# Kernel tuning notes

Hardware: AMD Instinct MI355X
Metric: run time of the kernel (lower is better)

Reference implementation:

```python
import jax, jax.numpy as jnp
import numpy as np

N, K, D, H, FF = 1024, 16, 512, 8, 2048
MUL_A, ES = 64, 64
E = N * K
HD = D // H          # vector channels per head
MH = MUL_A // H      # alpha channels per head
EPS = 1e-6


def smooth_lrelu(x, a=0.2):
    # SmoothLeakyReLU: (1+a)/2*x + (1-a)/2*x*(2*sigmoid(x)-1)
    return 0.5 * (1 + a) * x + 0.5 * (1 - a) * x * jnp.tanh(0.5 * x)


def vn_ln(x, g, b):
    # Vector-Neuron LayerNorm: LN over channel norms, rescale vectors.  x: [N, C, 3]
    n = jnp.sqrt(jnp.sum(x * x, axis=-1) + EPS)                  # [N, C]
    mu = n.mean(-1, keepdims=True)
    var = n.var(-1, keepdims=True)
    ln = (n - mu) / jnp.sqrt(var + EPS) * g + b
    return x / n[..., None] * ln[..., None]


def setup_inputs() -> dict:
    keys = iter(jax.random.split(jax.random.key(0), 40))
    def nrm(shape, scale=1.0):
        return jax.random.normal(next(keys), shape, jnp.float32) * scale
    d = {}
    d['tgt'] = nrm((N, 3 * D))
    d['memory'] = nrm((N, K, 3 * D))
    d['edge_sh'] = nrm((E, 4))
    d['edge_scalars'] = jax.random.uniform(next(keys), (E, ES), jnp.float32)
    sD = D ** -0.5
    d['W_src'] = nrm((D, D), sD)
    d['W_dst'] = nrm((D, D), sD)
    d['fc_w1'] = nrm((ES, 32), ES ** -0.5); d['fc_b1'] = jnp.zeros((32,), jnp.float32)
    d['fc_w2'] = nrm((32, 32), 32 ** -0.5); d['fc_b2'] = jnp.zeros((32,), jnp.float32)
    d['fc_w3'] = nrm((32, 3 * D), 32 ** -0.5); d['fc_b3'] = jnp.zeros((3 * D,), jnp.float32)
    d['W_alpha'] = nrm((D, MUL_A), sD)
    d['ln_a_g'] = jnp.ones((MUL_A,), jnp.float32)
    d['ln_a_b'] = jnp.zeros((MUL_A,), jnp.float32)
    d['alpha_dot'] = nrm((H, MH), MH ** -0.5)
    d['W_value'] = nrm((D, D), sD)
    d['W_proj'] = nrm((D, D), sD)
    d['n1_g'] = jnp.ones((D,), jnp.float32); d['n1_b'] = jnp.zeros((D,), jnp.float32)
    d['n2_g'] = jnp.ones((D,), jnp.float32); d['n2_b'] = jnp.zeros((D,), jnp.float32)
    d['W_ff1'] = nrm((FF, D), sD)
    d['W_ffd'] = nrm((FF, FF), FF ** -0.5)
    d['W_ff2'] = nrm((D, FF), FF ** -0.5)
    return d


def reference(tgt, memory, edge_sh, edge_scalars, W_src, W_dst,
              fc_w1, fc_b1, fc_w2, fc_b2, fc_w3, fc_b3,
              W_alpha, ln_a_g, ln_a_b, alpha_dot, W_value, W_proj,
              n1_g, n1_b, n2_g, n2_b, W_ff1, W_ffd, W_ff2):
    n, d3 = tgt.shape
    k = memory.shape[1]
    tv = jnp.einsum('oc,ncx->nox', W_dst, tgt.reshape(n, D, 3))          # linear_dst
    mv = jnp.einsum('oc,nkcx->nkox', W_src, memory.reshape(n, k, D, 3))  # linear_src
    msg = (tv[:, None] + mv).reshape(n * k, D, 3)                         # [E, D, 3]
    # radial MLP -> depthwise tensor-product weights
    h = jax.nn.silu(edge_scalars @ fc_w1 + fc_b1)
    h = jax.nn.silu(h @ fc_w2 + fc_b2)
    w = h @ fc_w3 + fc_b3                                                 # [E, 3D]
    w0, w1, w2 = jnp.split(w, 3, axis=-1)
    s = edge_sh[:, 0]
    v = edge_sh[:, 1:4]
    # depthwise TP with edge attr (1x0e+1x1e): 1e x 1e -> 0e, 1e x 0e -> 1e, 1e x 1e -> 1e
    p_sc = w0 * jnp.einsum('ecx,ex->ec', msg, v) / jnp.sqrt(3.0)          # [E, D]
    p_v1 = w1[:, :, None] * msg * s[:, None, None]                        # [E, D, 3]
    p_v2 = w2[:, :, None] * jnp.cross(msg, v[:, None, :]) / jnp.sqrt(2.0)
    # MLP attention on the invariant channel
    a = p_sc @ W_alpha                                                    # [E, MUL_A]
    a = (a - a.mean(-1, keepdims=True)) / jnp.sqrt(a.var(-1, keepdims=True) + EPS) * ln_a_g + ln_a_b
    a = smooth_lrelu(a).reshape(-1, H, MH)
    a = jnp.einsum('ehm,hm->eh', a, alpha_dot).reshape(n, k, H)
    a = jax.nn.softmax(a, axis=1)                                          # softmax over neighbors
    val = jnp.einsum('oc,ecx->eox', W_value, p_v1 + p_v2).reshape(n, k, H, HD, 3)
    out = jnp.einsum('nkh,nkhdx->nhdx', a, val).reshape(n, D, 3)
    out = jnp.einsum('oc,ncx->nox', W_proj, out)
    x = vn_ln(tv + out, n1_g, n1_b)
    # VN feed-forward: VNLinear -> VNLeakyReLU -> VNLinear
    y = jnp.einsum('oc,ncx->nox', W_ff1, x)                                # [N, FF, 3]
    dvec = jnp.einsum('oc,ncx->nox', W_ffd, y)
    dot = jnp.sum(y * dvec, -1)
    dnn = jnp.sum(dvec * dvec, -1) + EPS
    yproj = y - (dot / dnn)[..., None] * dvec
    y = jnp.where((dot >= 0)[..., None], y, 0.2 * y + 0.8 * yproj)
    y = jnp.einsum('oc,ncx->nox', W_ff2, y)
    x = vn_ln(x + y, n2_g, n2_b)
    return x.reshape(n, -1)
```

## Files before the change

### kernel.cpp

```cpp
#include <hip/hip_runtime.h>
#include <hip/hip_bf16.h>
#include <math.h>

#define EPS 1e-6f
#define RS3 0.57735026918962576f
#define RS2 0.70710678118654752f

typedef __attribute__((ext_vector_type(8))) short bf16x8;
typedef __attribute__((ext_vector_type(4))) float f32x4;

__device__ __forceinline__ ushort f2bf(float f) {
  unsigned u = __float_as_uint(f);
  u += 0x7fffu + ((u >> 16) & 1u);
  return (ushort)(u >> 16);
}
__device__ __forceinline__ float bf2f(ushort u) {
  return __uint_as_float(((unsigned)u) << 16);
}
__device__ __forceinline__ void split_hl(float v, ushort& h, ushort& l) {
  h = f2bf(v);
  l = f2bf(v - bf2f(h));
}
__device__ __forceinline__ float wave_sum64(float v) {
#pragma unroll
  for (int m = 32; m > 0; m >>= 1) v += __shfl_xor(v, m, 64);
  return v;
}

__global__ __launch_bounds__(256) void cvt_weights_hl(
    const float* __restrict__ w_src, const float* __restrict__ w_dst,
    const float* __restrict__ w_ff1, const float* __restrict__ w_ffd,
    const float* __restrict__ w_ff2, ushort* __restrict__ oh, ushort* __restrict__ ol)
{
  long i = ((long)blockIdx.x * 256 + threadIdx.x) * 8;
  const float* s; long l;
  if      (i < 262144)  { s = w_src; l = i; }
  else if (i < 524288)  { s = w_dst; l = i - 262144; }
  else if (i < 1572864) { s = w_ff1; l = i - 524288; }
  else if (i < 5767168) { s = w_ffd; l = i - 1572864; }
  else                  { s = w_ff2; l = i - 5767168; }
  ushort h[8], lo[8];
#pragma unroll
  for (int j = 0; j < 8; ++j) split_hl(s[l + j], h[j], lo[j]);
  ushort4 h0 = {h[0], h[1], h[2], h[3]}, h1 = {h[4], h[5], h[6], h[7]};
  ushort4 l0 = {lo[0], lo[1], lo[2], lo[3]}, l1 = {lo[4], lo[5], lo[6], lo[7]};
  *(ushort4*)(oh + i) = h0; *(ushort4*)(oh + i + 4) = h1;
  *(ushort4*)(ol + i) = l0; *(ushort4*)(ol + i + 4) = l1;
}

__global__ __launch_bounds__(256) void cvt_in_hl(
    const float* __restrict__ in, ushort* __restrict__ oh, ushort* __restrict__ ol)
{
  __shared__ float lds[6144];
  const int t = threadIdx.x;
  const long b0 = (long)blockIdx.x * 4;
  const float* ib = in + b0 * 1536;
#pragma unroll
  for (int r = 0; r < 6; ++r)
    *(float4*)(lds + r * 1024 + t * 4) = *(const float4*)(ib + r * 1024 + t * 4);
  __syncthreads();
#pragma unroll
  for (int r = 0; r < 24; ++r) {
    int l = t + 256 * r;
    int b = l >> 11, rem = l & 2047;
    b = l / 1536; rem = l - b * 1536;
    int x = rem >> 9, c = rem & 511;
    float v = lds[b * 1536 + c * 3 + x];
    ushort h, lo; split_hl(v, h, lo);
    oh[(b0 + b) * 1536 + rem] = h;
    ol[(b0 + b) * 1536 + rem] = lo;
  }
}

__global__ __launch_bounds__(256) void wcomb_kernel(
    const float* __restrict__ Wp, const float* __restrict__ Wv,
    ushort* __restrict__ oh, ushort* __restrict__ ol)
{
  __shared__ float wp[64 * 65];
  __shared__ float wv[64 * 65];
  const int h = blockIdx.x >> 3, ct = blockIdx.x & 7, pt = blockIdx.y;
  const int t = threadIdx.x;
#pragma unroll
  for (int r = 0; r < 16; ++r) {
    int f = r * 256 + t;
    int p = f >> 6, o = f & 63;
    wp[p * 65 + o] = Wp[(long)(pt * 64 + p) * 512 + h * 64 + o];
  }
#pragma unroll
  for (int r = 0; r < 16; ++r) {
    int f = r * 256 + t;
    int o = f >> 6, c = f & 63;
    wv[o * 65 + c] = Wv[(long)(h * 64 + o) * 512 + ct * 64 + c];
  }
  __syncthreads();
  const int tp = t >> 4, tc = t & 15;
  float acc[4][4] = {};
  for (int o = 0; o < 64; ++o) {
    float av[4], bv[4];
#pragma unroll
    for (int i = 0; i < 4; ++i) av[i] = wp[(tp * 4 + i) * 65 + o];
#pragma unroll
    for (int j = 0; j < 4; ++j) bv[j] = wv[o * 65 + tc * 4 + j];
#pragma unroll
    for (int i = 0; i < 4; ++i)
#pragma unroll
      for (int j = 0; j < 4; ++j) acc[i][j] += av[i] * bv[j];
  }
#pragma unroll
  for (int i = 0; i < 4; ++i) {
    int p = pt * 64 + tp * 4 + i;
    ushort h4[4], l4[4];
#pragma unroll
    for (int j = 0; j < 4; ++j) split_hl(acc[i][j], h4[j], l4[j]);
    ushort4 hv = {h4[0], h4[1], h4[2], h4[3]}, lv = {l4[0], l4[1], l4[2], l4[3]};
    long o = (long)p * 4096 + h * 512 + ct * 64 + tc * 4;
    *(ushort4*)(oh + o) = hv;
    *(ushort4*)(ol + o) = lv;
  }
}

template<int MT>
__global__ __launch_bounds__(256) void gemm_hl(
    const ushort* __restrict__ AH, const ushort* __restrict__ AL,
    const ushort* __restrict__ BH, const ushort* __restrict__ BL,
    float* __restrict__ Cf, ushort* __restrict__ CH, ushort* __restrict__ CL,
    const float* __restrict__ ADD, int M, int K, long bnp, int outmode)
{
  __shared__ __align__(16) ushort AsH[32 * MT * 72];
  __shared__ __align__(16) ushort AsL[32 * MT * 72];
  __shared__ __align__(16) ushort BsH[96 * 72];
  __shared__ __align__(16) ushort BsL[96 * 72];
  const int t = threadIdx.x;
  const int m0 = blockIdx.x * (32 * MT);
  const int j0 = blockIdx.y * 96;
  const int wid = t >> 6, lane = t & 63;
  const int wm = (wid >> 1) * (16 * MT), wn = (wid & 1) * 48;
  const int r16 = lane & 15, quad = lane >> 4;

  f32x4 acc[MT][3];
#pragma unroll
  for (int i = 0; i < MT; ++i)
#pragma unroll
    for (int j = 0; j < 3; ++j) acc[i][j] = (f32x4){0.f, 0.f, 0.f, 0.f};

  for (int k0 = 0; k0 < K; k0 += 64) {
#pragma unroll
    for (int r = 0; r < MT; ++r) {
      int f = r * 256 + t;
      int m = f >> 3, kc = f & 7;
      long off = (long)(m0 + m) * K + k0 + kc * 8;
      *(uint4*)(AsH + m * 72 + kc * 8) = *(const uint4*)(AH + off);
      *(uint4*)(AsL + m * 72 + kc * 8) = *(const uint4*)(AL + off);
    }
#pragma unroll
    for (int r = 0; r < 3; ++r) {
      int f = r * 256 + t;
      int n = f >> 3, kc = f & 7;
      int jj = j0 + n;
      int bq = jj / 3, xr = jj - bq * 3;
      long off = (long)bq * bnp + (long)xr * K + k0 + kc * 8;
      *(uint4*)(BsH + n * 72 + kc * 8) = *(const uint4*)(BH + off);
      *(uint4*)(BsL + n * 72 + kc * 8) = *(const uint4*)(BL + off);
    }
    __syncthreads();
#pragma unroll
    for (int kh = 0; kh < 2; ++kh) {
      bf16x8 ah[MT], al[MT], bh[3], bl[3];
#pragma unroll
      for (int i = 0; i < MT; ++i) {
        int ro = (wm + i * 16 + r16) * 72 + kh * 32 + quad * 8;
        ah[i] = *(const bf16x8*)(AsH + ro);
        al[i] = *(const bf16x8*)(AsL + ro);
      }
#pragma unroll
      for (int j = 0; j < 3; ++j) {
        int ro = (wn + j * 16 + r16) * 72 + kh * 32 + quad * 8;
        bh[j] = *(const bf16x8*)(BsH + ro);
        bl[j] = *(const bf16x8*)(BsL + ro);
      }
#pragma unroll
      for (int i = 0; i < MT; ++i)
#pragma unroll
        for (int j = 0; j < 3; ++j) {
          acc[i][j] = __builtin_amdgcn_mfma_f32_16x16x32_bf16(ah[i], bh[j], acc[i][j], 0, 0, 0);
          acc[i][j] = __builtin_amdgcn_mfma_f32_16x16x32_bf16(ah[i], bl[j], acc[i][j], 0, 0, 0);
          acc[i][j] = __builtin_amdgcn_mfma_f32_16x16x32_bf16(al[i], bh[j], acc[i][j], 0, 0, 0);
        }
    }
    __syncthreads();
  }

#pragma unroll
  for (int j = 0; j < 3; ++j) {
    int jj = j0 + wn + j * 16 + r16;
    const float* ap = ADD ? (ADD + (long)(jj / 48) * 1536 + (jj % 3) * 512) : nullptr;
#pragma unroll
    for (int i = 0; i < MT; ++i) {
      int mm = m0 + wm + i * 16 + quad * 4;
      f32x4 v = acc[i][j];
      if (ap) { v.x += ap[mm]; v.y += ap[mm + 1]; v.z += ap[mm + 2]; v.w += ap[mm + 3]; }
      long o = (long)jj * M + mm;
      if (outmode != 1) *(f32x4*)(Cf + o) = v;
      if (outmode != 0) {
        ushort h[4], l[4];
        split_hl(v.x, h[0], l[0]); split_hl(v.y, h[1], l[1]);
        split_hl(v.z, h[2], l[2]); split_hl(v.w, h[3], l[3]);
        ushort4 hv = {h[0], h[1], h[2], h[3]}, lv = {l[0], l[1], l[2], l[3]};
        *(ushort4*)(CH + o) = hv;
        *(ushort4*)(CL + o) = lv;
      }
    }
  }
}

__global__ __launch_bounds__(256) void edge_kernel(
    ushort* __restrict__ msgH, ushort* __restrict__ msgL,
    const float* __restrict__ edge_sh, const float* __restrict__ edge_scalars,
    const float* __restrict__ fc_w1, const float* __restrict__ fc_b1,
    const float* __restrict__ fc_w2, const float* __restrict__ fc_b2,
    const float* __restrict__ fc_w3, const float* __restrict__ fc_b3,
    const float* __restrict__ W_alpha, const float* __restrict__ ln_g,
    const float* __restrict__ ln_b, const float* __restrict__ alpha_dot,
    float* __restrict__ logits)
{
  __shared__ float esl[4][64];
  __shared__ float h1l[4][32];
  __shared__ float h2l[4][32];
  __shared__ float shl[4][4];
  __shared__ float pscl[4][512];
  __shared__ float smem_big[4 * 1536];

  const int t = threadIdx.x;
  const int e0 = blockIdx.x * 4;
  const int W1O = 0, W2O = 2048, B1O = 3072, B2O = 3104;

  { int el = t >> 6, i = t & 63;
    esl[el][i] = edge_scalars[(long)(e0 + el) * 64 + i]; }
  if (t < 16) shl[t >> 2][t & 3] = edge_sh[(long)e0 * 4 + t];
#pragma unroll
  for (int r = 0; r < 13; ++r) {
    int l = t + 256 * r;
    if (l < 2048)      smem_big[W1O + l] = fc_w1[l];
    else if (l < 3072) smem_big[W2O + (l - 2048)] = fc_w2[l - 2048];
    else if (l < 3104) smem_big[B1O + (l - 3072)] = fc_b1[l - 3072];
    else if (l < 3136) smem_big[B2O + (l - 3104)] = fc_b2[l - 3104];
  }
  __syncthreads();

  if (t < 128) {
    int el = t >> 5, j = t & 31;
    float v = smem_big[B1O + j];
#pragma unroll 8
    for (int i = 0; i < 64; ++i) v += esl[el][i] * smem_big[W1O + i * 32 + j];
    h1l[el][j] = v / (1.f + expf(-v));
  }
  __syncthreads();
  if (t < 128) {
    int el = t >> 5, j = t & 31;
    float v = smem_big[B2O + j];
#pragma unroll 8
    for (int i = 0; i < 32; ++i) v += h1l[el][i] * smem_big[W2O + i * 32 + j];
    h2l[el][j] = v / (1.f + expf(-v));
  }
  __syncthreads();

  {
    float wacc[4][6];
#pragma unroll
    for (int q = 0; q < 6; ++q) {
      float b3 = fc_b3[t + 256 * q];
#pragma unroll
      for (int el = 0; el < 4; ++el) wacc[el][q] = b3;
    }
#pragma unroll 4
    for (int j = 0; j < 32; ++j) {
      float h2e[4];
#pragma unroll
      for (int el = 0; el < 4; ++el) h2e[el] = h2l[el][j];
#pragma unroll
      for (int q = 0; q < 6; ++q) {
        float w3 = fc_w3[j * 1536 + t + 256 * q];
#pragma unroll
        for (int el = 0; el < 4; ++el) wacc[el][q] += h2e[el] * w3;
      }
    }
    __syncthreads();
#pragma unroll
    for (int q = 0; q < 6; ++q)
#pragma unroll
      for (int el = 0; el < 4; ++el)
        smem_big[el * 1536 + t + 256 * q] = wacc[el][q];
  }
  __syncthreads();

  const int el = t >> 6, lane = t & 63;
  const long ebase = (long)(e0 + el) * 1536;
  const float s  = shl[el][0], vx = shl[el][1], vy = shl[el][2], vz = shl[el][3];
  const float* wle = smem_big + el * 1536;

#pragma unroll
  for (int i = 0; i < 8; ++i) {
    int c = lane + 64 * i;
    float m0 = bf2f(msgH[ebase + c])        + bf2f(msgL[ebase + c]);
    float m1 = bf2f(msgH[ebase + 512 + c])  + bf2f(msgL[ebase + 512 + c]);
    float m2 = bf2f(msgH[ebase + 1024 + c]) + bf2f(msgL[ebase + 1024 + c]);
    float w0 = wle[c], w1 = wle[512 + c], w2 = wle[1024 + c];
    float dotv = m0 * vx + m1 * vy + m2 * vz;
    pscl[el][c] = w0 * dotv * RS3;
    float cx = m1 * vz - m2 * vy;
    float cy = m2 * vx - m0 * vz;
    float cz = m0 * vy - m1 * vx;
    float f1 = w1 * s;
    float f2 = w2 * RS2;
    float p0 = f1 * m0 + f2 * cx;
    float p1 = f1 * m1 + f2 * cy;
    float p2 = f1 * m2 + f2 * cz;
    ushort h, lo;
    split_hl(p0, h, lo); msgH[ebase + c] = h;        msgL[ebase + c] = lo;
    split_hl(p1, h, lo); msgH[ebase + 512 + c] = h;  msgL[ebase + 512 + c] = lo;
    split_hl(p2, h, lo); msgH[ebase + 1024 + c] = h; msgL[ebase + 1024 + c] = lo;
  }
  __syncthreads();

  float accm = 0.f;
  for (int ch = 0; ch < 8; ++ch) {
#pragma unroll
    for (int r = 0; r < 16; ++r) {
      int l = t + 256 * r;
      smem_big[l] = W_alpha[(long)(ch * 64) * 64 + l];
    }
    __syncthreads();
#pragma unroll 8
    for (int cl = 0; cl < 64; ++cl)
      accm += pscl[el][ch * 64 + cl] * smem_big[cl * 64 + lane];
    __syncthreads();
  }

  float s1 = wave_sum64(accm);
  float s2 = wave_sum64(accm * accm);
  float mu  = s1 * (1.f / 64.f);
  float var = s2 * (1.f / 64.f) - mu * mu;
  float aln = (accm - mu) * rsqrtf(var + EPS) * ln_g[lane] + ln_b[lane];
  float act = 0.6f * aln + 0.4f * aln * tanhf(0.5f * aln);
  float p = act * alpha_dot[lane];
#pragma unroll
  for (int d2 = 4; d2 > 0; d2 >>= 1) p += __shfl_down(p, d2, 8);
  if ((lane & 7) == 0) logits[(long)(e0 + el) * 8 + (lane >> 3)] = p;
}

__global__ __launch_bounds__(256) void attn_agg(
    const float* __restrict__ logits, ushort* __restrict__ pvH, ushort* __restrict__ pvL)
{
  __shared__ float atl[16][8];
  const int n = blockIdx.x, t = threadIdx.x;
  if (t < 128) {
    int k = t >> 3, h = t & 7;
    atl[k][h] = logits[((long)n * 16 + k) * 8 + h];
  }
  __syncthreads();
  if (t < 8) {
    int h = t;
    float mx = -1e30f;
    for (int k = 0; k < 16; ++k) mx = fmaxf(mx, atl[k][h]);
    float ex[16]; float sm = 0.f;
    for (int k = 0; k < 16; ++k) { ex[k] = expf(atl[k][h] - mx); sm += ex[k]; }
    float inv = 1.f / sm;
    for (int k = 0; k < 16; ++k) atl[k][h] = ex[k] * inv;
  }
  __syncthreads();

  float acc[6][8];
#pragma unroll
  for (int i = 0; i < 6; ++i)
#pragma unroll
    for (int h = 0; h < 8; ++h) acc[i][h] = 0.f;

  const long sb = (long)n * 24576;
  for (int k = 0; k < 16; ++k) {
    float aw[8];
#pragma unroll
    for (int h = 0; h < 8; ++h) aw[h] = atl[k][h];
#pragma unroll
    for (int i = 0; i < 6; ++i) {
      long off = sb + k * 1536 + t + 256 * i;
      float mval = bf2f(pvH[off]) + bf2f(pvL[off]);
#pragma unroll
      for (int h = 0; h < 8; ++h) acc[i][h] += aw[h] * mval;
    }
  }
  __syncthreads();
#pragma unroll
  for (int i = 0; i < 6; ++i) {
    int l = t + 256 * i;
    int x = l >> 9, c = l & 511;
#pragma unroll
    for (int h = 0; h < 8; ++h) {
      ushort hh, ll; split_hl(acc[i][h], hh, ll);
      long off = sb + x * 4096 + h * 512 + c;
      pvH[off] = hh; pvL[off] = ll;
    }
  }
}

__global__ __launch_bounds__(256) void vn_ln_x(
    const float* __restrict__ A, const float* __restrict__ Bp,
    const float* __restrict__ g, const float* __restrict__ bb,
    float* __restrict__ outf, ushort* __restrict__ outH, ushort* __restrict__ outL,
    int mode)
{
  const int n = blockIdx.x, t = threadIdx.x;
  const long base = (long)n * 1536;
  float xv[2][3], nrm[2];
#pragma unroll
  for (int q = 0; q < 2; ++q) {
    int c = t + 256 * q;
    float ssq = 0.f;
#pragma unroll
    for (int x = 0; x < 3; ++x) {
      float v = A[base + x * 512 + c] + Bp[base + x * 512 + c];
      xv[q][x] = v; ssq += v * v;
    }
    nrm[q] = sqrtf(ssq + EPS);
  }
  float s1 = nrm[0] + nrm[1];
  float s2 = nrm[0] * nrm[0] + nrm[1] * nrm[1];
  s1 = wave_sum64(s1); s2 = wave_sum64(s2);
  __shared__ float red[8];
  int wid = t >> 6;
  if ((t & 63) == 0) { red[wid] = s1; red[4 + wid] = s2; }
  __syncthreads();
  float S1 = red[0] + red[1] + red[2] + red[3];
  float S2 = red[4] + red[5] + red[6] + red[7];
  float mu  = S1 * (1.f / 512.f);
  float var = S2 * (1.f / 512.f) - mu * mu;
  float rstd = rsqrtf(var + EPS);
#pragma unroll
  for (int q = 0; q < 2; ++q) {
    int c = t + 256 * q;
    float ln = (nrm[q] - mu) * rstd * g[c] + bb[c];
    float sc = ln / nrm[q];
    if (mode == 0) {
#pragma unroll
      for (int x = 0; x < 3; ++x) {
        float v = xv[q][x] * sc;
        outf[base + x * 512 + c] = v;
        ushort h, lo; split_hl(v, h, lo);
        outH[base + x * 512 + c] = h;
        outL[base + x * 512 + c] = lo;
      }
    } else {
#pragma unroll
      for (int x = 0; x < 3; ++x)
        outf[base + c * 3 + x] = xv[q][x] * sc;
    }
  }
}

__global__ __launch_bounds__(256) void gate_hl(
    const float* __restrict__ y, const float* __restrict__ dv,
    ushort* __restrict__ gh, ushort* __restrict__ gl)
{
  long idx = (long)blockIdx.x * 256 + threadIdx.x;
  long n = idx >> 11; int o = idx & 2047;
  long b = n * 6144 + o;
  float y0 = y[b], y1 = y[b + 2048], y2 = y[b + 4096];
  float d0 = dv[b], d1 = dv[b + 2048], d2 = dv[b + 4096];
  float dot = y0 * d0 + y1 * d1 + y2 * d2;
  if (dot < 0.f) {
    float dnn = d0 * d0 + d1 * d1 + d2 * d2 + EPS;
    float coef = 0.8f * dot / dnn;
    y0 -= coef * d0; y1 -= coef * d1; y2 -= coef * d2;
  }
  ushort h, lo;
  split_hl(y0, h, lo); gh[b] = h;        gl[b] = lo;
  split_hl(y1, h, lo); gh[b + 2048] = h; gl[b + 2048] = lo;
  split_hl(y2, h, lo); gh[b + 4096] = h; gl[b + 4096] = lo;
}

extern "C" void kernel_launch(void* const* d_in, const int* in_sizes, int n_in,
                              void* d_out, int out_size, void* d_ws, size_t ws_size,
                              hipStream_t stream)
{
  const float* tgt          = (const float*)d_in[0];
  const float* memory       = (const float*)d_in[1];
  const float* edge_sh      = (const float*)d_in[2];
  const float* edge_scalars = (const float*)d_in[3];
  const float* W_src   = (const float*)d_in[4];
  const float* W_dst   = (const float*)d_in[5];
  const float* fc_w1   = (const float*)d_in[6];
  const float* fc_b1   = (const float*)d_in[7];
  const float* fc_w2   = (const float*)d_in[8];
  const float* fc_b2   = (const float*)d_in[9];
  const float* fc_w3   = (const float*)d_in[10];
  const float* fc_b3   = (const float*)d_in[11];
  const float* W_alpha = (const float*)d_in[12];
  const float* ln_a_g  = (const float*)d_in[13];
  const float* ln_a_b  = (const float*)d_in[14];
  const float* alpha_dot = (const float*)d_in[15];
  const float* W_value = (const float*)d_in[16];
  const float* W_proj  = (const float*)d_in[17];
  const float* n1_g    = (const float*)d_in[18];
  const float* n1_b    = (const float*)d_in[19];
  const float* n2_g    = (const float*)d_in[20];
  const float* n2_b    = (const float*)d_in[21];
  const float* W_ff1   = (const float*)d_in[22];
  const float* W_ffd   = (const float*)d_in[23];
  const float* W_ff2   = (const float*)d_in[24];
  float* out = (float*)d_out;

  char* ws = (char*)d_ws;
  ushort* msgH = (ushort*)(ws + 0);
  ushort* msgL = (ushort*)(ws + 50331648);
  float*  yf   = (float*)(ws + 0);
  ushort* yH   = (ushort*)(ws + 25165824);
  ushort* yL   = (ushort*)(ws + 37748736);
  float*  dvf  = (float*)(ws + 50331648);
  ushort* gyH  = (ushort*)(ws + 75497472);
  ushort* gyL  = (ushort*)(ws + 88080384);
  float*  tvx  = (float*)(ws + 100663296);
  float*  nb2  = (float*)(ws + 106954752);
  ushort* tgtH  = (ushort*)(ws + 113246208);
  ushort* tgtL  = (ushort*)(ws + 116391936);
  ushort* memcH = (ushort*)(ws + 113246208);
  ushort* memcL = (ushort*)(ws + 119537664);
  float*  x1f   = (float*)(ws + 113246208);
  ushort* x1H   = (ushort*)(ws + 119537664);
  ushort* x1L   = (ushort*)(ws + 122683392);
  float*  logits = (float*)(ws + 125829120);
  ushort* WH    = (ushort*)(ws + 126353408);
  ushort* WL    = (ushort*)(ws + 139984896);
  ushort* wcH   = (ushort*)(ws + 153616384);
  ushort* wcL   = (ushort*)(ws + 157810688);

  const long SRC = 0, DST = 262144, FF1 = 524288, FFD = 1572864, FF2 = 5767168;

  cvt_weights_hl<<<3328, 256, 0, stream>>>(W_src, W_dst, W_ff1, W_ffd, W_ff2, WH, WL);
  wcomb_kernel<<<dim3(64, 8), 256, 0, stream>>>(W_proj, W_value, wcH, wcL);

  cvt_in_hl<<<256, 256, 0, stream>>>(tgt, tgtH, tgtL);
  gemm_hl<2><<<dim3(8, 32), 256, 0, stream>>>(WH + DST, WL + DST, tgtH, tgtL,
      tvx, nullptr, nullptr, nullptr, 512, 512, 1536, 0);

  for (int q = 0; q < 8; ++q) {
    cvt_in_hl<<<512, 256, 0, stream>>>(memory + (long)q * 2048 * 1536, memcH, memcL);
    gemm_hl<4><<<dim3(4, 64), 256, 0, stream>>>(WH + SRC, WL + SRC, memcH, memcL,
        nullptr, msgH + (long)q * 3145728, msgL + (long)q * 3145728,
        tvx + (long)q * 196608, 512, 512, 1536, 1);
  }

  edge_kernel<<<4096, 256, 0, stream>>>(msgH, msgL, edge_sh, edge_scalars,
      fc_w1, fc_b1, fc_w2, fc_b2, fc_w3, fc_b3, W_alpha, ln_a_g, ln_a_b, alpha_dot, logits);

  attn_agg<<<1024, 256, 0, stream>>>(logits, msgH, msgL);

  gemm_hl<2><<<dim3(8, 32), 256, 0, stream>>>(wcH, wcL, msgH, msgL,
      nb2, nullptr, nullptr, nullptr, 512, 4096, 24576, 0);

  vn_ln_x<<<1024, 256, 0, stream>>>(tvx, nb2, n1_g, n1_b, x1f, x1H, x1L, 0);

  gemm_hl<4><<<dim3(16, 32), 256, 0, stream>>>(WH + FF1, WL + FF1, x1H, x1L,
      yf, yH, yL, nullptr, 2048, 512, 1536, 2);

  gemm_hl<4><<<dim3(16, 32), 256, 0, stream>>>(WH + FFD, WL + FFD, yH, yL,
      dvf, nullptr, nullptr, nullptr, 2048, 2048, 6144, 0);

  gate_hl<<<8192, 256, 0, stream>>>(yf, dvf, gyH, gyL);

  gemm_hl<2><<<dim3(8, 32), 256, 0, stream>>>(WH + FF2, WL + FF2, gyH, gyL,
      nb2, nullptr, nullptr, nullptr, 512, 2048, 6144, 0);

  vn_ln_x<<<1024, 256, 0, stream>>>(x1f, nb2, n2_g, n2_b, out, nullptr, nullptr, 1);
}
```

Before: 901.1 us.

## Fuse input bf16 split into GEMM loads and merge edge and attention kernels

Adds a GEMM variant that reads fp32 tgt/memory directly, transposes and splits to bf16 hi/lo while staging into LDS. This removes the separate cvt_in_hl passes and the 8-way chunked loop over memory. The edge kernel and attention aggregation are merged into one kernel per node (16 edges per block). Messages stay in registers, which avoids writing them back and rereading them. The cost is heavy register use (wacc[16][6], pvr[16][6]) with one block per SM, strided uncoalesced B loads in the GEMM, and a serial 512-step W_alpha loop per wave.

After: 1.309 ms. 1.45x slower.

```diff
diff --git a/kernel.cpp b/kernel.cpp
--- a/kernel.cpp
+++ b/kernel.cpp
@@ -46,30 +46,6 @@
   ushort4 l0 = {lo[0], lo[1], lo[2], lo[3]}, l1 = {lo[4], lo[5], lo[6], lo[7]};
   *(ushort4*)(oh + i) = h0; *(ushort4*)(oh + i + 4) = h1;
   *(ushort4*)(ol + i) = l0; *(ushort4*)(ol + i + 4) = l1;
-}
-
-__global__ __launch_bounds__(256) void cvt_in_hl(
-    const float* __restrict__ in, ushort* __restrict__ oh, ushort* __restrict__ ol)
-{
-  __shared__ float lds[6144];
-  const int t = threadIdx.x;
-  const long b0 = (long)blockIdx.x * 4;
-  const float* ib = in + b0 * 1536;
-#pragma unroll
-  for (int r = 0; r < 6; ++r)
-    *(float4*)(lds + r * 1024 + t * 4) = *(const float4*)(ib + r * 1024 + t * 4);
-  __syncthreads();
-#pragma unroll
-  for (int r = 0; r < 24; ++r) {
-    int l = t + 256 * r;
-    int b = l >> 11, rem = l & 2047;
-    b = l / 1536; rem = l - b * 1536;
-    int x = rem >> 9, c = rem & 511;
-    float v = lds[b * 1536 + c * 3 + x];
-    ushort h, lo; split_hl(v, h, lo);
-    oh[(b0 + b) * 1536 + rem] = h;
-    ol[(b0 + b) * 1536 + rem] = lo;
-  }
 }
 
 __global__ __launch_bounds__(256) void wcomb_kernel(
@@ -213,193 +189,291 @@
   }
 }
 
-__global__ __launch_bounds__(256) void edge_kernel(
+template<int MT>
+__global__ __launch_bounds__(256) void gemm_hlf(
+    const ushort* __restrict__ AH, const ushort* __restrict__ AL,
+    const float* __restrict__ Bf,
+    float* __restrict__ Cf, ushort* __restrict__ CH, ushort* __restrict__ CL,
+    const float* __restrict__ ADD, int M, int K, int outmode)
+{
+  __shared__ __align__(16) ushort AsH[32 * MT * 72];
+  __shared__ __align__(16) ushort AsL[32 * MT * 72];
+  __shared__ __align__(16) ushort BsH[96 * 72];
+  __shared__ __align__(16) ushort BsL[96 * 72];
+  const int t = threadIdx.x;
+  const int m0 = blockIdx.x * (32 * MT);
+  const int j0 = blockIdx.y * 96;
+  const int wid = t >> 6, lane = t & 63;
+  const int wm = (wid >> 1) * (16 * MT), wn = (wid & 1) * 48;
+  const int r16 = lane & 15, quad = lane >> 4;
+
+  f32x4 acc[MT][3];
+#pragma unroll
+  for (int i = 0; i < MT; ++i)
+#pragma unroll
+    for (int j = 0; j < 3; ++j) acc[i][j] = (f32x4){0.f, 0.f, 0.f, 0.f};
+
+  for (int k0 = 0; k0 < K; k0 += 64) {
+#pragma unroll
+    for (int r = 0; r < MT; ++r) {
+      int f = r * 256 + t;
+      int m = f >> 3, kc = f & 7;
+      long off = (long)(m0 + m) * K + k0 + kc * 8;
+      *(uint4*)(AsH + m * 72 + kc * 8) = *(const uint4*)(AH + off);
+      *(uint4*)(AsL + m * 72 + kc * 8) = *(const uint4*)(AL + off);
+    }
+#pragma unroll
+    for (int r = 0; r < 3; ++r) {
+      int f = r * 256 + t;
+      int n = f >> 3, kc = f & 7;
+      int jj = j0 + n;
+      int bq = jj / 3, xr = jj - bq * 3;
+      const float* bp = Bf + (long)bq * (3 * K) + (long)(k0 + kc * 8) * 3 + xr;
+      ushort hh[8], ll[8];
+#pragma unroll
+      for (int i = 0; i < 8; ++i) split_hl(bp[i * 3], hh[i], ll[i]);
+      *(ushort4*)(BsH + n * 72 + kc * 8)     = *(ushort4*)hh;
+      *(ushort4*)(BsH + n * 72 + kc * 8 + 4) = *(ushort4*)(hh + 4);
+      *(ushort4*)(BsL + n * 72 + kc * 8)     = *(ushort4*)ll;
+      *(ushort4*)(BsL + n * 72 + kc * 8 + 4) = *(ushort4*)(ll + 4);
+    }
+    __syncthreads();
+#pragma unroll
+    for (int kh = 0; kh < 2; ++kh) {
+      bf16x8 ah[MT], al[MT], bh[3], bl[3];
+#pragma unroll
+      for (int i = 0; i < MT; ++i) {
+        int ro = (wm + i * 16 + r16) * 72 + kh * 32 + quad * 8;
+        ah[i] = *(const bf16x8*)(AsH + ro);
+        al[i] = *(const bf16x8*)(AsL + ro);
+      }
+#pragma unroll
+      for (int j = 0; j < 3; ++j) {
+        int ro = (wn + j * 16 + r16) * 72 + kh * 32 + quad * 8;
+        bh[j] = *(const bf16x8*)(BsH + ro);
+        bl[j] = *(const bf16x8*)(BsL + ro);
+      }
+#pragma unroll
+      for (int i = 0; i < MT; ++i)
+#pragma unroll
+        for (int j = 0; j < 3; ++j) {
+          acc[i][j] = __builtin_amdgcn_mfma_f32_16x16x32_bf16(ah[i], bh[j], acc[i][j], 0, 0, 0);
+          acc[i][j] = __builtin_amdgcn_mfma_f32_16x16x32_bf16(ah[i], bl[j], acc[i][j], 0, 0, 0);
+          acc[i][j] = __builtin_amdgcn_mfma_f32_16x16x32_bf16(al[i], bh[j], acc[i][j], 0, 0, 0);
+        }
+    }
+    __syncthreads();
+  }
+
+#pragma unroll
+  for (int j = 0; j < 3; ++j) {
+    int jj = j0 + wn + j * 16 + r16;
+    const float* ap = ADD ? (ADD + (long)(jj / 48) * 1536 + (jj % 3) * 512) : nullptr;
+#pragma unroll
+    for (int i = 0; i < MT; ++i) {
+      int mm = m0 + wm + i * 16 + quad * 4;
+      f32x4 v = acc[i][j];
+      if (ap) { v.x += ap[mm]; v.y += ap[mm + 1]; v.z += ap[mm + 2]; v.w += ap[mm + 3]; }
+      long o = (long)jj * M + mm;
+      if (outmode != 1) *(f32x4*)(Cf + o) = v;
+      if (outmode != 0) {
+        ushort h[4], l[4];
+        split_hl(v.x, h[0], l[0]); split_hl(v.y, h[1], l[1]);
+        split_hl(v.z, h[2], l[2]); split_hl(v.w, h[3], l[3]);
+        ushort4 hv = {h[0], h[1], h[2], h[3]}, lv = {l[0], l[1], l[2], l[3]};
+        *(ushort4*)(CH + o) = hv;
+        *(ushort4*)(CL + o) = lv;
+      }
+    }
+  }
+}
+
+__global__ __launch_bounds__(256, 1) void edge_attn(
     ushort* __restrict__ msgH, ushort* __restrict__ msgL,
     const float* __restrict__ edge_sh, const float* __restrict__ edge_scalars,
     const float* __restrict__ fc_w1, const float* __restrict__ fc_b1,
     const float* __restrict__ fc_w2, const float* __restrict__ fc_b2,
     const float* __restrict__ fc_w3, const float* __restrict__ fc_b3,
     const float* __restrict__ W_alpha, const float* __restrict__ ln_g,
-    const float* __restrict__ ln_b, const float* __restrict__ alpha_dot,
-    float* __restrict__ logits)
-{
-  __shared__ float esl[4][64];
-  __shared__ float h1l[4][32];
-  __shared__ float h2l[4][32];
-  __shared__ float shl[4][4];
-  __shared__ float pscl[4][512];
-  __shared__ float smem_big[4 * 1536];
+    const float* __restrict__ ln_b, const float* __restrict__ alpha_dot)
+{
+  __shared__ float w_all[16 * 1536];
+  __shared__ float psc[16 * 512];
+  __shared__ float esl[16 * 64];
+  __shared__ float h1l[16 * 32];
+  __shared__ float h2l[16 * 32];
+  __shared__ float shl[16 * 4];
+  __shared__ float atl[16 * 8];
 
   const int t = threadIdx.x;
-  const int e0 = blockIdx.x * 4;
-  const int W1O = 0, W2O = 2048, B1O = 3072, B2O = 3104;
-
-  { int el = t >> 6, i = t & 63;
-    esl[el][i] = edge_scalars[(long)(e0 + el) * 64 + i]; }
-  if (t < 16) shl[t >> 2][t & 3] = edge_sh[(long)e0 * 4 + t];
+  const int n = blockIdx.x;
+  const int e0 = n * 16;
+  const int lane = t & 63, wvi = t >> 6;
+
+#pragma unroll
+  for (int r = 0; r < 4; ++r)
+    esl[t + 256 * r] = edge_scalars[(long)e0 * 64 + t + 256 * r];
+  if (t < 64) shl[t] = edge_sh[(long)e0 * 4 + t];
 #pragma unroll
   for (int r = 0; r < 13; ++r) {
     int l = t + 256 * r;
-    if (l < 2048)      smem_big[W1O + l] = fc_w1[l];
-    else if (l < 3072) smem_big[W2O + (l - 2048)] = fc_w2[l - 2048];
-    else if (l < 3104) smem_big[B1O + (l - 3072)] = fc_b1[l - 3072];
-    else if (l < 3136) smem_big[B2O + (l - 3104)] = fc_b2[l - 3104];
-  }
-  __syncthreads();
-
-  if (t < 128) {
-    int el = t >> 5, j = t & 31;
-    float v = smem_big[B1O + j];
+    if (l < 2048)      psc[l] = fc_w1[l];
+    else if (l < 3072) psc[l] = fc_w2[l - 2048];
+    else if (l < 3104) psc[l] = fc_b1[l - 3072];
+    else if (l < 3136) psc[l] = fc_b2[l - 3104];
+  }
+  __syncthreads();
+
+#pragma unroll
+  for (int it = 0; it < 2; ++it) {
+    int l = t + 256 * it;
+    int e = l >> 5, j = l & 31;
+    float v = psc[3072 + j];
 #pragma unroll 8
-    for (int i = 0; i < 64; ++i) v += esl[el][i] * smem_big[W1O + i * 32 + j];
-    h1l[el][j] = v / (1.f + expf(-v));
-  }
-  __syncthreads();
-  if (t < 128) {
-    int el = t >> 5, j = t & 31;
-    float v = smem_big[B2O + j];
+    for (int i = 0; i < 64; ++i) v += esl[e * 64 + i] * psc[i * 32 + j];
+    h1l[e * 32 + j] = v / (1.f + expf(-v));
+  }
+  __syncthreads();
+#pragma unroll
+  for (int it = 0; it < 2; ++it) {
+    int l = t + 256 * it;
+    int e = l >> 5, j = l & 31;
+    float v = psc[3104 + j];
 #pragma unroll 8
-    for (int i = 0; i < 32; ++i) v += h1l[el][i] * smem_big[W2O + i * 32 + j];
-    h2l[el][j] = v / (1.f + expf(-v));
+    for (int i = 0; i < 32; ++i) v += h1l[e * 32 + i] * psc[2048 + i * 32 + j];
+    h2l[e * 32 + j] = v / (1.f + expf(-v));
   }
   __syncthreads();
 
   {
-    float wacc[4][6];
+    float wacc[16][6];
 #pragma unroll
     for (int q = 0; q < 6; ++q) {
       float b3 = fc_b3[t + 256 * q];
 #pragma unroll
-      for (int el = 0; el < 4; ++el) wacc[el][q] = b3;
-    }
-#pragma unroll 4
+      for (int e = 0; e < 16; ++e) wacc[e][q] = b3;
+    }
     for (int j = 0; j < 32; ++j) {
-      float h2e[4];
-#pragma unroll
-      for (int el = 0; el < 4; ++el) h2e[el] = h2l[el][j];
-#pragma unroll
-      for (int q = 0; q < 6; ++q) {
-        float w3 = fc_w3[j * 1536 + t + 256 * q];
-#pragma unroll
-        for (int el = 0; el < 4; ++el) wacc[el][q] += h2e[el] * w3;
-      }
-    }
-    __syncthreads();
-#pragma unroll
-    for (int q = 0; q < 6; ++q)
-#pragma unroll
-      for (int el = 0; el < 4; ++el)
-        smem_big[el * 1536 + t + 256 * q] = wacc[el][q];
-  }
-  __syncthreads();
-
-  const int el = t >> 6, lane = t & 63;
-  const long ebase = (long)(e0 + el) * 1536;
-  const float s  = shl[el][0], vx = shl[el][1], vy = shl[el][2], vz = shl[el][3];
-  const float* wle = smem_big + el * 1536;
-
-#pragma unroll
-  for (int i = 0; i < 8; ++i) {
-    int c = lane + 64 * i;
-    float m0 = bf2f(msgH[ebase + c])        + bf2f(msgL[ebase + c]);
-    float m1 = bf2f(msgH[ebase + 512 + c])  + bf2f(msgL[ebase + 512 + c]);
-    float m2 = bf2f(msgH[ebase + 1024 + c]) + bf2f(msgL[ebase + 1024 + c]);
-    float w0 = wle[c], w1 = wle[512 + c], w2 = wle[1024 + c];
-    float dotv = m0 * vx + m1 * vy + m2 * vz;
-    pscl[el][c] = w0 * dotv * RS3;
-    float cx = m1 * vz - m2 * vy;
-    float cy = m2 * vx - m0 * vz;
-    float cz = m0 * vy - m1 * vx;
-    float f1 = w1 * s;
-    float f2 = w2 * RS2;
-    float p0 = f1 * m0 + f2 * cx;
-    float p1 = f1 * m1 + f2 * cy;
-    float p2 = f1 * m2 + f2 * cz;
-    ushort h, lo;
-    split_hl(p0, h, lo); msgH[ebase + c] = h;        msgL[ebase + c] = lo;
-    split_hl(p1, h, lo); msgH[ebase + 512 + c] = h;  msgL[ebase + 512 + c] = lo;
-    split_hl(p2, h, lo); msgH[ebase + 1024 + c] = h; msgL[ebase + 1024 + c] = lo;
-  }
-  __syncthreads();
-
-  float accm = 0.f;
-  for (int ch = 0; ch < 8; ++ch) {
-#pragma unroll
-    for (int r = 0; r < 16; ++r) {
-      int l = t + 256 * r;
-      smem_big[l] = W_alpha[(long)(ch * 64) * 64 + l];
-    }
-    __syncthreads();
+      float w3[6];
+#pragma unroll
+      for (int q = 0; q < 6; ++q) w3[q] = fc_w3[j * 1536 + t + 256 * q];
+#pragma unroll
+      for (int e = 0; e < 16; ++e) {
+        float h2 = h2l[e * 32 + j];
+#pragma unroll
+        for (int q = 0; q < 6; ++q) wacc[e][q] += h2 * w3[q];
+      }
+    }
+#pragma unroll
+    for (int e = 0; e < 16; ++e)
+#pragma unroll
+      for (int q = 0; q < 6; ++q)
+        w_all[e * 1536 + t + 256 * q] = wacc[e][q];
+  }
+  __syncthreads();
+
+  const int c0 = t * 2;
+  float pvr[16][6];
+#pragma unroll
+  for (int k = 0; k < 16; ++k) {
+    const long eb = (long)(e0 + k) * 1536;
+    const float s  = shl[k * 4 + 0], vx = shl[k * 4 + 1],
+                vy = shl[k * 4 + 2], vz = shl[k * 4 + 3];
+    float2 w0p = *(const float2*)&w_all[k * 1536 + c0];
+    float2 w1p = *(const float2*)&w_all[k * 1536 + 512 + c0];
+    float2 w2p = *(const float2*)&w_all[k * 1536 + 1024 + c0];
+    float pout[2];
+#pragma unroll
+    for (int ci = 0; ci < 2; ++ci) {
+      int c = c0 + ci;
+      float m0 = bf2f(msgH[eb + c])        + bf2f(msgL[eb + c]);
+      float m1 = bf2f(msgH[eb + 512 + c])  + bf2f(msgL[eb + 512 + c]);
+      float m2 = bf2f(msgH[eb + 1024 + c]) + bf2f(msgL[eb + 1024 + c]);
+      float w0 = ci ? w0p.y : w0p.x;
+      float w1 = ci ? w1p.y : w1p.x;
+      float w2 = ci ? w2p.y : w2p.x;
+      float dotv = m0 * vx + m1 * vy + m2 * vz;
+      pout[ci] = w0 * dotv * RS3;
+      float cx = m1 * vz - m2 * vy;
+      float cy = m2 * vx - m0 * vz;
+      float cz = m0 * vy - m1 * vx;
+      float f1 = w1 * s, f2 = w2 * RS2;
+      pvr[k][ci * 3 + 0] = f1 * m0 + f2 * cx;
+      pvr[k][ci * 3 + 1] = f1 * m1 + f2 * cy;
+      pvr[k][ci * 3 + 2] = f1 * m2 + f2 * cz;
+    }
+    *(float2*)&psc[k * 512 + c0] = make_float2(pout[0], pout[1]);
+  }
+  __syncthreads();
+
+  {
+    float accm[4] = {0.f, 0.f, 0.f, 0.f};
+    const int kb = wvi * 4;
 #pragma unroll 8
-    for (int cl = 0; cl < 64; ++cl)
-      accm += pscl[el][ch * 64 + cl] * smem_big[cl * 64 + lane];
-    __syncthreads();
-  }
-
-  float s1 = wave_sum64(accm);
-  float s2 = wave_sum64(accm * accm);
-  float mu  = s1 * (1.f / 64.f);
-  float var = s2 * (1.f / 64.f) - mu * mu;
-  float aln = (accm - mu) * rsqrtf(var + EPS) * ln_g[lane] + ln_b[lane];
-  float act = 0.6f * aln + 0.4f * aln * tanhf(0.5f * aln);
-  float p = act * alpha_dot[lane];
-#pragma unroll
-  for (int d2 = 4; d2 > 0; d2 >>= 1) p += __shfl_down(p, d2, 8);
-  if ((lane & 7) == 0) logits[(long)(e0 + el) * 8 + (lane >> 3)] = p;
-}
-
-__global__ __launch_bounds__(256) void attn_agg(
-    const float* __restrict__ logits, ushort* __restrict__ pvH, ushort* __restrict__ pvL)
-{
-  __shared__ float atl[16][8];
-  const int n = blockIdx.x, t = threadIdx.x;
-  if (t < 128) {
-    int k = t >> 3, h = t & 7;
-    atl[k][h] = logits[((long)n * 16 + k) * 8 + h];
-  }
-  __syncthreads();
+    for (int c = 0; c < 512; ++c) {
+      float wa = W_alpha[c * 64 + lane];
+#pragma unroll
+      for (int q = 0; q < 4; ++q) accm[q] += psc[(kb + q) * 512 + c] * wa;
+    }
+    float lg = ln_g[lane], lb = ln_b[lane], ad = alpha_dot[lane];
+#pragma unroll
+    for (int q = 0; q < 4; ++q) {
+      float a = accm[q];
+      float s1 = wave_sum64(a);
+      float s2 = wave_sum64(a * a);
+      float mu  = s1 * (1.f / 64.f);
+      float var = s2 * (1.f / 64.f) - mu * mu;
+      float aln = (a - mu) * rsqrtf(var + EPS) * lg + lb;
+      float act = 0.6f * aln + 0.4f * aln * tanhf(0.5f * aln);
+      float p = act * ad;
+#pragma unroll
+      for (int d2 = 4; d2 > 0; d2 >>= 1) p += __shfl_down(p, d2, 8);
+      if ((lane & 7) == 0) atl[(kb + q) * 8 + (lane >> 3)] = p;
+    }
+  }
+  __syncthreads();
+
   if (t < 8) {
     int h = t;
     float mx = -1e30f;
-    for (int k = 0; k < 16; ++k) mx = fmaxf(mx, atl[k][h]);
-    float ex[16]; float sm = 0.f;
-    for (int k = 0; k < 16; ++k) { ex[k] = expf(atl[k][h] - mx); sm += ex[k]; }
+    for (int k = 0; k < 16; ++k) mx = fmaxf(mx, atl[k * 8 + h]);
+    float ex[16], sm = 0.f;
+    for (int k = 0; k < 16; ++k) { ex[k] = expf(atl[k * 8 + h] - mx); sm += ex[k]; }
     float inv = 1.f / sm;
-    for (int k = 0; k < 16; ++k) atl[k][h] = ex[k] * inv;
-  }
-  __syncthreads();
-
-  float acc[6][8];
-#pragma unroll
-  for (int i = 0; i < 6; ++i)
-#pragma unroll
-    for (int h = 0; h < 8; ++h) acc[i][h] = 0.f;
-
-  const long sb = (long)n * 24576;
+    for (int k = 0; k < 16; ++k) atl[k * 8 + h] = ex[k] * inv;
+  }
+  __syncthreads();
+
+  float agg[8][6];
+#pragma unroll
+  for (int h = 0; h < 8; ++h)
+#pragma unroll
+    for (int q = 0; q < 6; ++q) agg[h][q] = 0.f;
+#pragma unroll
   for (int k = 0; k < 16; ++k) {
     float aw[8];
 #pragma unroll
-    for (int h = 0; h < 8; ++h) aw[h] = atl[k][h];
-#pragma unroll
-    for (int i = 0; i < 6; ++i) {
-      long off = sb + k * 1536 + t + 256 * i;
-      float mval = bf2f(pvH[off]) + bf2f(pvL[off]);
-#pragma unroll
-      for (int h = 0; h < 8; ++h) acc[i][h] += aw[h] * mval;
-    }
-  }
-  __syncthreads();
-#pragma unroll
-  for (int i = 0; i < 6; ++i) {
-    int l = t + 256 * i;
-    int x = l >> 9, c = l & 511;
+    for (int h = 0; h < 8; ++h) aw[h] = atl[k * 8 + h];
+#pragma unroll
+    for (int h = 0; h < 8; ++h)
+#pragma unroll
+      for (int q = 0; q < 6; ++q) agg[h][q] += aw[h] * pvr[k][q];
+  }
+
+  const long ob = (long)n * 24576;
+#pragma unroll
+  for (int x = 0; x < 3; ++x)
 #pragma unroll
     for (int h = 0; h < 8; ++h) {
-      ushort hh, ll; split_hl(acc[i][h], hh, ll);
-      long off = sb + x * 4096 + h * 512 + c;
-      pvH[off] = hh; pvL[off] = ll;
-    }
-  }
+      float v0 = agg[h][x], v1 = agg[h][3 + x];
+      ushort h0, l0, h1, l1;
+      split_hl(v0, h0, l0); split_hl(v1, h1, l1);
+      long o = ob + x * 4096 + h * 512 + c0;
+      ushort2 uh; uh.x = h0; uh.y = h1;
+      ushort2 ul; ul.x = l0; ul.y = l1;
+      *(ushort2*)(msgH + o) = uh;
+      *(ushort2*)(msgL + o) = ul;
+    }
 }
 
 __global__ __launch_bounds__(256) void vn_ln_x(
@@ -519,14 +593,9 @@
   ushort* gyL  = (ushort*)(ws + 88080384);
   float*  tvx  = (float*)(ws + 100663296);
   float*  nb2  = (float*)(ws + 106954752);
-  ushort* tgtH  = (ushort*)(ws + 113246208);
-  ushort* tgtL  = (ushort*)(ws + 116391936);
-  ushort* memcH = (ushort*)(ws + 113246208);
-  ushort* memcL = (ushort*)(ws + 119537664);
   float*  x1f   = (float*)(ws + 113246208);
   ushort* x1H   = (ushort*)(ws + 119537664);
   ushort* x1L   = (ushort*)(ws + 122683392);
-  float*  logits = (float*)(ws + 125829120);
   ushort* WH    = (ushort*)(ws + 126353408);
   ushort* WL    = (ushort*)(ws + 139984896);
   ushort* wcH   = (ushort*)(ws + 153616384);
@@ -537,21 +606,14 @@
   cvt_weights_hl<<<3328, 256, 0, stream>>>(W_src, W_dst, W_ff1, W_ffd, W_ff2, WH, WL);
   wcomb_kernel<<<dim3(64, 8), 256, 0, stream>>>(W_proj, W_value, wcH, wcL);
 
-  cvt_in_hl<<<256, 256, 0, stream>>>(tgt, tgtH, tgtL);
-  gemm_hl<2><<<dim3(8, 32), 256, 0, stream>>>(WH + DST, WL + DST, tgtH, tgtL,
-      tvx, nullptr, nullptr, nullptr, 512, 512, 1536, 0);
-
-  for (int q = 0; q < 8; ++q) {
-    cvt_in_hl<<<512, 256, 0, stream>>>(memory + (long)q * 2048 * 1536, memcH, memcL);
-    gemm_hl<4><<<dim3(4, 64), 256, 0, stream>>>(WH + SRC, WL + SRC, memcH, memcL,
-        nullptr, msgH + (long)q * 3145728, msgL + (long)q * 3145728,
-        tvx + (long)q * 196608, 512, 512, 1536, 1);
-  }
-
-  edge_kernel<<<4096, 256, 0, stream>>>(msgH, msgL, edge_sh, edge_scalars,
-      fc_w1, fc_b1, fc_w2, fc_b2, fc_w3, fc_b3, W_alpha, ln_a_g, ln_a_b, alpha_dot, logits);
-
-  attn_agg<<<1024, 256, 0, stream>>>(logits, msgH, msgL);
+  gemm_hlf<2><<<dim3(8, 32), 256, 0, stream>>>(WH + DST, WL + DST, tgt,
+      tvx, nullptr, nullptr, nullptr, 512, 512, 0);
+
+  gemm_hlf<4><<<dim3(4, 512), 256, 0, stream>>>(WH + SRC, WL + SRC, memory,
+      nullptr, msgH, msgL, tvx, 512, 512, 1);
+
+  edge_attn<<<1024, 256, 0, stream>>>(msgH, msgL, edge_sh, edge_scalars,
+      fc_w1, fc_b1, fc_w2, fc_b2, fc_w3, fc_b3, W_alpha, ln_a_g, ln_a_b, alpha_dot);
 
   gemm_hl<2><<<dim3(8, 32), 256, 0, stream>>>(wcH, wcL, msgH, msgL,
       nb2, nullptr, nullptr, nullptr, 512, 4096, 24576, 0);
```
